# Kernel tuning notes

Hardware: AMD Instinct MI355X
Metric: run time of the kernel (lower is better)

The kernel has to match this reference:

```python
import jax, jax.numpy as jnp
import numpy as np

FACTOR = 5  # init factor


def setup_inputs() -> dict:
    key = jax.random.key(0)
    k1, k2, k3, k4 = jax.random.split(key, 4)
    B, H, L, D = 4, 8, 2048, 64
    sample_k = min(FACTOR * int(np.ceil(np.log(L))), L)  # 40
    queries = jax.random.normal(k1, (B, H, L, D), dtype=jnp.float32)
    keys = jax.random.normal(k2, (B, H, L, D), dtype=jnp.float32)
    values = jax.random.normal(k3, (B, H, L, D), dtype=jnp.float32)
    index_sample = jax.random.randint(k4, (L, sample_k), 0, L)
    return {"queries": queries, "keys": keys, "values": values,
            "index_sample": index_sample}


def reference(queries, keys, values, index_sample):
    B, H, L_Q, D = queries.shape
    L_K = keys.shape[2]
    n_top = min(FACTOR * int(np.ceil(np.log(L_Q))), L_Q)

    # --- _prob_QK ---
    # Gather sampled keys per query position: [B,H,L_Q,sample_k,D]
    K_sample = keys[:, :, index_sample, :]
    # Q.unsqueeze(3) @ K_sample^T -> [B,H,L_Q,sample_k]
    Q_K_sample = jnp.einsum('bhld,bhlsd->bhls', queries, K_sample)
    # sparsity measure M = max - mean
    M = Q_K_sample.max(axis=-1) - Q_K_sample.sum(axis=-1) / L_K
    _, M_top = jax.lax.top_k(M, n_top)  # [B,H,n_top]
    # gather top queries: [B,H,n_top,D]
    Q_reduce = jnp.take_along_axis(queries, M_top[..., None], axis=2)
    # full scores for top queries: [B,H,n_top,L_K]
    scores_top = jnp.einsum('bhud,bhkd->bhuk', Q_reduce, keys)

    # --- scale ---
    scale = 1.0 / np.sqrt(D).astype(np.float32)
    scores_top = scores_top * scale

    # --- initial context (mask_flag=False): mean of V broadcast over L_Q ---
    V_mean = values.mean(axis=2)  # [B,H,D]
    context = jnp.broadcast_to(V_mean[:, :, None, :], (B, H, L_Q, D))

    # --- update context at top-query positions ---
    attn = jax.nn.softmax(scores_top, axis=-1)           # [B,H,n_top,L_K]
    ctx_update = jnp.einsum('bhuk,bhkd->bhud', attn, values)
    b_idx = jnp.arange(B)[:, None, None]
    h_idx = jnp.arange(H)[None, :, None]
    context = context.at[b_idx, h_idx, M_top].set(ctx_update)
    return context
```

## Files before the change

### kernel.cpp

```cpp
#include <hip/hip_runtime.h>
#include <math.h>

#define BH 32
#define L  2048
#define D  64
#define SK 40
#define NT 40
#define NC 16
#define CK 128
#define SP 129
#define SCALE 0.125f

#define WS_M      0
#define WS_MTOP   262144
#define WS_VP     267264
#define WS_VM     529408
#define WS_QTOP   537600
#define WS_OPART  865280
#define WS_MPART  6108160
#define WS_LPART  6190080

template <int CTRL>
__device__ __forceinline__ float dpp_add(float x) {
    int y = __builtin_amdgcn_update_dpp(0, __float_as_int(x), CTRL, 0xF, 0xF, true);
    return x + __int_as_float(y);
}

__global__ __launch_bounds__(512) void kMV(const float* __restrict__ Q,
                                           const float* __restrict__ K,
                                           const float* __restrict__ V,
                                           const int* __restrict__ idx,
                                           float* __restrict__ M,
                                           float* __restrict__ Vp)
{
    __shared__ int   sidx[64 * SK];
    __shared__ float red[512];

    int t    = threadIdx.x;
    int b    = blockIdx.x;
    int head = ((b >> 3) & 3) * 8 + (b & 7);
    int qc   = b >> 5;
    int l0   = qc * 64;

    {
        int d = t & 63, r = t >> 6;
        const float* Vb = V + ((size_t)head * L + l0 + r * 8) * D + d;
        float acc = 0.f;
        #pragma unroll
        for (int k = 0; k < 8; ++k) acc += Vb[(size_t)k * D];
        red[t] = acc;
    }
    for (int i = t; i < 64 * SK; i += 512) sidx[i] = idx[l0 * SK + i];
    __syncthreads();
    if (t < 64) {
        float s = 0.f;
        #pragma unroll
        for (int rr = 0; rr < 8; ++rr) s += red[t + rr * 64];
        Vp[(head * 32 + qc) * 64 + t] = s;
    }

    int wave = t >> 6, lane = t & 63;
    int g  = lane >> 3;
    int dl = lane & 7;
    int lq = wave * 8 + g;
    size_t qid = (size_t)head * L + (l0 + lq);

    const float4* Q4 = reinterpret_cast<const float4*>(Q);
    float4 q0 = Q4[qid * 16 + dl * 2 + 0];
    float4 q1 = Q4[qid * 16 + dl * 2 + 1];
    const float4* Kb4 = reinterpret_cast<const float4*>(K) + (size_t)head * L * 16;

    const int* sp = sidx + lq * SK;

    float4 ka[4], kb[4];
    #pragma unroll
    for (int s = 0; s < 4; ++s) {
        const float4* kp = Kb4 + ((sp[s] << 4) + (dl << 1));
        ka[s] = kp[0]; kb[s] = kp[1];
    }
    float mx = -INFINITY, sm = 0.f;
    #pragma unroll
    for (int s = 0; s < SK; ++s) {
        float4 k0 = ka[s & 3], k1 = kb[s & 3];
        if (s + 4 < SK) {
            const float4* kp = Kb4 + ((sp[s + 4] << 4) + (dl << 1));
            ka[s & 3] = kp[0]; kb[s & 3] = kp[1];
        }
        float p = q0.x * k0.x + q0.y * k0.y + q0.z * k0.z + q0.w * k0.w
                + q1.x * k1.x + q1.y * k1.y + q1.z * k1.z + q1.w * k1.w;
        p = dpp_add<0xB1>(p);
        p = dpp_add<0x4E>(p);
        p = dpp_add<0x12C>(p);
        mx = fmaxf(mx, p);
        sm += p;
    }
    if (dl == 0) M[qid] = mx - sm * (1.0f / (float)L);
}

__global__ __launch_bounds__(256) void kTopVm(const float* __restrict__ M,
                                              const float* __restrict__ Vp,
                                              const float* __restrict__ Q,
                                              int* __restrict__ Mtop,
                                              float* __restrict__ Vm,
                                              float* __restrict__ Qtop)
{
    __shared__ unsigned int keys[L];
    __shared__ int hist[256];
    __shared__ int wtot[4];
    __shared__ unsigned int pref_s;
    __shared__ int krem_s;
    __shared__ int cnt_gt, cnt_eq;
    __shared__ int eqlist[64];
    __shared__ int stop[NT];

    int bh = blockIdx.x;
    int t  = threadIdx.x;
    int lane = t & 63, w = t >> 6;

    if (t < 64) {
        float s = 0.f;
        #pragma unroll
        for (int c = 0; c < 32; ++c) s += Vp[(bh * 32 + c) * 64 + t];
        Vm[bh * D + t] = s * (1.0f / (float)L);
    }

    for (int i = t; i < L; i += 256) {
        unsigned int u = __float_as_uint(M[bh * L + i]);
        keys[i] = (u & 0x80000000u) ? ~u : (u | 0x80000000u);
    }
    if (t == 0) { pref_s = 0u; krem_s = NT; cnt_gt = 0; cnt_eq = 0; }
    __syncthreads();

    #pragma unroll
    for (int shift = 24; shift >= 0; shift -= 8) {
        hist[t] = 0;
        __syncthreads();
        unsigned int pref = pref_s;
        int krem = krem_s;
        for (int i = t; i < L; i += 256) {
            unsigned int k  = keys[i];
            unsigned int hi = (shift == 24) ? 0u : (k >> (shift + 8));
            if (hi == pref) atomicAdd(&hist[(k >> shift) & 0xFF], 1);
        }
        __syncthreads();
        int h = hist[t];
        int v = h;
        #pragma unroll
        for (int o = 1; o < 64; o <<= 1) {
            int u = __shfl_down(v, o, 64);
            if (lane + o < 64) v += u;
        }
        if (lane == 0) wtot[w] = v;
        __syncthreads();
        int ss = v;
        #pragma unroll
        for (int w2 = 1; w2 < 4; ++w2) if (w2 > w) ss += wtot[w2];
        if (ss - h < krem && ss >= krem) {
            krem_s = krem - (ss - h);
            pref_s = (pref << 8) | (unsigned int)t;
        }
    }
    __syncthreads();

    unsigned int T = pref_s;
    int krem = krem_s;
    for (int i = t; i < L; i += 256) {
        unsigned int k = keys[i];
        if (k > T) {
            int p = atomicAdd(&cnt_gt, 1);
            Mtop[bh * NT + p] = i;
            stop[p] = i;
        } else if (k == T) {
            int p = atomicAdd(&cnt_eq, 1);
            if (p < 64) eqlist[p] = i;
        }
    }
    __syncthreads();
    if (t == 0) {
        int base = cnt_gt;
        int m = cnt_eq < 64 ? cnt_eq : 64;
        for (int q = 0; q < krem; ++q) {
            int best = 0x7fffffff, bj = -1;
            for (int j = 0; j < m; ++j) if (eqlist[j] < best) { best = eqlist[j]; bj = j; }
            Mtop[bh * NT + base + q] = best;
            stop[base + q] = best;
            if (bj >= 0) eqlist[bj] = 0x7fffffff;
        }
    }
    __syncthreads();
    const float4* Qg = reinterpret_cast<const float4*>(Q) + (size_t)bh * L * 16;
    float4* Qt = reinterpret_cast<float4*>(Qtop) + (size_t)bh * NT * 16;
    for (int i = t; i < NT * 16; i += 256)
        Qt[i] = Qg[(size_t)stop[i >> 4] * 16 + (i & 15)];
}

__global__ __launch_bounds__(256, 2) void kAttnPart(const float* __restrict__ Qtop,
                                                    const float* __restrict__ K,
                                                    const float* __restrict__ V,
                                                    const float* __restrict__ Vm,
                                                    float* __restrict__ Opart,
                                                    float* __restrict__ mpart,
                                                    float* __restrict__ lpart,
                                                    float* __restrict__ out)
{
    __shared__ float4 V4[CK * 16];
    __shared__ float  S[NT * SP];
    __shared__ float  smax[NT], ssum[NT];

    int c = blockIdx.x, bh = blockIdx.y;
    int t = threadIdx.x;

    {
        const float4* Vm4 = reinterpret_cast<const float4*>(Vm + bh * D);
        float4* outB = reinterpret_cast<float4*>(out) + ((size_t)bh * L + c * CK) * 16;
        #pragma unroll
        for (int k = 0; k < 8; ++k) { int i = t + k * 256; outB[i] = Vm4[i & 15]; }
    }

    const float4* Vg = reinterpret_cast<const float4*>(V) + ((size_t)bh * L + c * CK) * 16;
    float4 vreg[8];
    #pragma unroll
    for (int k = 0; k < 8; ++k) vreg[k] = Vg[t + k * 256];

    int w    = __builtin_amdgcn_readfirstlane(t) >> 6;
    int lane = t & 63;
    const float4* Kg = reinterpret_cast<const float4*>(K) + ((size_t)bh * L + c * CK) * 16;
    float4 k0[16], k1[16];
    #pragma unroll
    for (int d4 = 0; d4 < 16; ++d4) {
        k0[d4] = Kg[(size_t)lane * 16 + d4];
        k1[d4] = Kg[(size_t)(64 + lane) * 16 + d4];
    }

    const float* Qb = Qtop + ((size_t)bh * NT + w * 10) * D;
    float p0[10], p1[10];
    #pragma unroll
    for (int i = 0; i < 10; ++i) {
        const float* qrow = Qb + i * D;
        float a0 = 0.f, a1 = 0.f;
        #pragma unroll
        for (int d4 = 0; d4 < 16; ++d4) {
            float4 q4 = *reinterpret_cast<const float4*>(qrow + d4 * 4);
            a0 += q4.x * k0[d4].x + q4.y * k0[d4].y + q4.z * k0[d4].z + q4.w * k0[d4].w;
            a1 += q4.x * k1[d4].x + q4.y * k1[d4].y + q4.z * k1[d4].z + q4.w * k1[d4].w;
        }
        p0[i] = a0 * SCALE; p1[i] = a1 * SCALE;
    }

    #pragma unroll
    for (int i = 0; i < 10; ++i) {
        int u = w * 10 + i;
        float m = fmaxf(p0[i], p1[i]);
        #pragma unroll
        for (int o = 1; o < 64; o <<= 1) m = fmaxf(m, __shfl_xor(m, o, 64));
        float e0 = __expf(p0[i] - m), e1 = __expf(p1[i] - m);
        float l2 = e0 + e1;
        #pragma unroll
        for (int o = 1; o < 64; o <<= 1) l2 += __shfl_xor(l2, o, 64);
        S[u * SP + lane]      = e0;
        S[u * SP + 64 + lane] = e1;
        if (lane == 0) { smax[u] = m; ssum[u] = l2; }
    }

    #pragma unroll
    for (int k = 0; k < 8; ++k) {
        int i = t + k * 256;
        int j = i >> 4, d4 = i & 15;
        V4[j * 16 + (d4 ^ (j & 15))] = vreg[k];
    }
    __syncthreads();

    {
        int a = t >> 5, r = t & 31;
        int d4 = r >> 1, jh = r & 1;
        float4 acc[5];
        #pragma unroll
        for (int ui = 0; ui < 5; ++ui) acc[ui] = make_float4(0.f, 0.f, 0.f, 0.f);
        for (int jj = 0; jj < 64; ++jj) {
            int j = jh * 64 + jj;
            float4 v4 = V4[j * 16 + (d4 ^ (j & 15))];
            #pragma unroll
            for (int ui = 0; ui < 5; ++ui) {
                float p = S[(a + 8 * ui) * SP + j];
                acc[ui].x += p * v4.x; acc[ui].y += p * v4.y;
                acc[ui].z += p * v4.z; acc[ui].w += p * v4.w;
            }
        }
        #pragma unroll
        for (int ui = 0; ui < 5; ++ui) {
            acc[ui].x = dpp_add<0xB1>(acc[ui].x);
            acc[ui].y = dpp_add<0xB1>(acc[ui].y);
            acc[ui].z = dpp_add<0xB1>(acc[ui].z);
            acc[ui].w = dpp_add<0xB1>(acc[ui].w);
        }
        if (jh == 0) {
            float4* Og = reinterpret_cast<float4*>(Opart) + ((size_t)(bh * NC + c) * NT) * 16;
            #pragma unroll
            for (int ui = 0; ui < 5; ++ui)
                Og[(a + 8 * ui) * 16 + d4] = acc[ui];
        }
    }
    if (t < NT) {
        mpart[(bh * NC + c) * NT + t] = smax[t];
        lpart[(bh * NC + c) * NT + t] = ssum[t];
    }
}

__global__ __launch_bounds__(64) void kCombine(const float* __restrict__ Opart,
                                               const float* __restrict__ mpart,
                                               const float* __restrict__ lpart,
                                               const int* __restrict__ Mtop,
                                               float* __restrict__ out)
{
    int u = blockIdx.x, bh = blockIdx.y, d = threadIdx.x;
    float gm = -INFINITY, den = 0.f, o = 0.f;
    for (int c = 0; c < NC; ++c) {
        int pi = (bh * NC + c) * NT + u;
        float mv = mpart[pi], lv = lpart[pi];
        float nm = fmaxf(gm, mv);
        float r1 = __expf(gm - nm), r2 = __expf(mv - nm);
        o   = o * r1 + r2 * Opart[(size_t)pi * D + d];
        den = den * r1 + r2 * lv;
        gm  = nm;
    }
    int qrow = Mtop[bh * NT + u];
    out[((size_t)bh * L + qrow) * D + d] = o / den;
}

extern "C" void kernel_launch(void* const* d_in, const int* in_sizes, int n_in,
                              void* d_out, int out_size, void* d_ws, size_t ws_size,
                              hipStream_t stream)
{
    const float* Q   = (const float*)d_in[0];
    const float* K   = (const float*)d_in[1];
    const float* V   = (const float*)d_in[2];
    const int*   idx = (const int*)d_in[3];
    float* out = (float*)d_out;

    char* ws = (char*)d_ws;
    float* M     = (float*)(ws + WS_M);
    int*   Mtop  = (int*)  (ws + WS_MTOP);
    float* Vp    = (float*)(ws + WS_VP);
    float* Vm    = (float*)(ws + WS_VM);
    float* Qtop  = (float*)(ws + WS_QTOP);
    float* Opart = (float*)(ws + WS_OPART);
    float* mpart = (float*)(ws + WS_MPART);
    float* lpart = (float*)(ws + WS_LPART);

    kMV      <<<1024, 512, 0, stream>>>(Q, K, V, idx, M, Vp);
    kTopVm   <<<BH, 256, 0, stream>>>(M, Vp, Q, Mtop, Vm, Qtop);
    kAttnPart<<<dim3(NC, BH), 256, 0, stream>>>(Qtop, K, V, Vm, Opart, mpart, lpart, out);
    kCombine <<<dim3(NT, BH), 64, 0, stream>>>(Opart, mpart, lpart, Mtop, out);
}
```

Measured before the change: 186.9 us.

## Halve attention chunk size to double split-K blocks and simplify combine

The key chunk per attention block drops from 128 to 64 keys, so twice as many blocks run, each holding fewer registers, and the occupancy hint is removed. The combine kernel now finds the global max first and then sums weighted partials in one unrolled pass, instead of doing an online rescale at every step. The sampled-score kernel drops its manual 4-deep software prefetch in favour of a plain loop unrolled by 4. The cost is twice as many partial outputs to write and to read back during the combine.

```diff
diff --git a/kernel.cpp b/kernel.cpp
--- a/kernel.cpp
+++ b/kernel.cpp
@@ -6,9 +6,9 @@
 #define D  64
 #define SK 40
 #define NT 40
-#define NC 16
-#define CK 128
-#define SP 129
+#define NC 32
+#define CK 64
+#define SP 65
 #define SCALE 0.125f
 
 #define WS_M      0
@@ -17,8 +17,8 @@
 #define WS_VM     529408
 #define WS_QTOP   537600
 #define WS_OPART  865280
-#define WS_MPART  6108160
-#define WS_LPART  6190080
+#define WS_MPART  11351040
+#define WS_LPART  11514880
 
 template <int CTRL>
 __device__ __forceinline__ float dpp_add(float x) {
@@ -70,22 +70,12 @@
     float4 q1 = Q4[qid * 16 + dl * 2 + 1];
     const float4* Kb4 = reinterpret_cast<const float4*>(K) + (size_t)head * L * 16;
 
-    const int* sp = sidx + lq * SK;
-
-    float4 ka[4], kb[4];
-    #pragma unroll
-    for (int s = 0; s < 4; ++s) {
-        const float4* kp = Kb4 + ((sp[s] << 4) + (dl << 1));
-        ka[s] = kp[0]; kb[s] = kp[1];
-    }
     float mx = -INFINITY, sm = 0.f;
-    #pragma unroll
+    #pragma unroll 4
     for (int s = 0; s < SK; ++s) {
-        float4 k0 = ka[s & 3], k1 = kb[s & 3];
-        if (s + 4 < SK) {
-            const float4* kp = Kb4 + ((sp[s + 4] << 4) + (dl << 1));
-            ka[s & 3] = kp[0]; kb[s & 3] = kp[1];
-        }
+        int kr = sidx[lq * SK + s];
+        const float4* kp = Kb4 + (size_t)kr * 16 + dl * 2;
+        float4 k0 = kp[0], k1 = kp[1];
         float p = q0.x * k0.x + q0.y * k0.y + q0.z * k0.z + q0.w * k0.w
                 + q1.x * k1.x + q1.y * k1.y + q1.z * k1.z + q1.w * k1.w;
         p = dpp_add<0xB1>(p);
@@ -194,16 +184,16 @@
         Qt[i] = Qg[(size_t)stop[i >> 4] * 16 + (i & 15)];
 }
 
-__global__ __launch_bounds__(256, 2) void kAttnPart(const float* __restrict__ Qtop,
-                                                    const float* __restrict__ K,
-                                                    const float* __restrict__ V,
-                                                    const float* __restrict__ Vm,
-                                                    float* __restrict__ Opart,
-                                                    float* __restrict__ mpart,
-                                                    float* __restrict__ lpart,
-                                                    float* __restrict__ out)
-{
-    __shared__ float4 V4[CK * 16];
+__global__ __launch_bounds__(256) void kAttnPart(const float* __restrict__ Qtop,
+                                                 const float* __restrict__ K,
+                                                 const float* __restrict__ V,
+                                                 const float* __restrict__ Vm,
+                                                 float* __restrict__ Opart,
+                                                 float* __restrict__ mpart,
+                                                 float* __restrict__ lpart,
+                                                 float* __restrict__ out)
+{
+    __shared__ float4 V4s[CK * 16];
     __shared__ float  S[NT * SP];
     __shared__ float  smax[NT], ssum[NT];
 
@@ -214,59 +204,53 @@
         const float4* Vm4 = reinterpret_cast<const float4*>(Vm + bh * D);
         float4* outB = reinterpret_cast<float4*>(out) + ((size_t)bh * L + c * CK) * 16;
         #pragma unroll
-        for (int k = 0; k < 8; ++k) { int i = t + k * 256; outB[i] = Vm4[i & 15]; }
+        for (int k = 0; k < 4; ++k) { int i = t + k * 256; outB[i] = Vm4[i & 15]; }
     }
 
     const float4* Vg = reinterpret_cast<const float4*>(V) + ((size_t)bh * L + c * CK) * 16;
-    float4 vreg[8];
-    #pragma unroll
-    for (int k = 0; k < 8; ++k) vreg[k] = Vg[t + k * 256];
+    float4 vreg[4];
+    #pragma unroll
+    for (int k = 0; k < 4; ++k) vreg[k] = Vg[t + k * 256];
 
     int w    = __builtin_amdgcn_readfirstlane(t) >> 6;
     int lane = t & 63;
     const float4* Kg = reinterpret_cast<const float4*>(K) + ((size_t)bh * L + c * CK) * 16;
-    float4 k0[16], k1[16];
-    #pragma unroll
-    for (int d4 = 0; d4 < 16; ++d4) {
-        k0[d4] = Kg[(size_t)lane * 16 + d4];
-        k1[d4] = Kg[(size_t)(64 + lane) * 16 + d4];
-    }
-
-    const float* Qb = Qtop + ((size_t)bh * NT + w * 10) * D;
-    float p0[10], p1[10];
+    float4 k[16];
+    #pragma unroll
+    for (int d4 = 0; d4 < 16; ++d4) k[d4] = Kg[(size_t)lane * 16 + d4];
+
+    const float4* Qb = reinterpret_cast<const float4*>(Qtop) + ((size_t)bh * NT + w * 10) * 16;
+    float p[10];
     #pragma unroll
     for (int i = 0; i < 10; ++i) {
-        const float* qrow = Qb + i * D;
-        float a0 = 0.f, a1 = 0.f;
+        float a0 = 0.f;
         #pragma unroll
         for (int d4 = 0; d4 < 16; ++d4) {
-            float4 q4 = *reinterpret_cast<const float4*>(qrow + d4 * 4);
-            a0 += q4.x * k0[d4].x + q4.y * k0[d4].y + q4.z * k0[d4].z + q4.w * k0[d4].w;
-            a1 += q4.x * k1[d4].x + q4.y * k1[d4].y + q4.z * k1[d4].z + q4.w * k1[d4].w;
-        }
-        p0[i] = a0 * SCALE; p1[i] = a1 * SCALE;
+            float4 q4 = Qb[i * 16 + d4];
+            a0 += q4.x * k[d4].x + q4.y * k[d4].y + q4.z * k[d4].z + q4.w * k[d4].w;
+        }
+        p[i] = a0 * SCALE;
     }
 
     #pragma unroll
     for (int i = 0; i < 10; ++i) {
         int u = w * 10 + i;
-        float m = fmaxf(p0[i], p1[i]);
+        float m = p[i];
         #pragma unroll
         for (int o = 1; o < 64; o <<= 1) m = fmaxf(m, __shfl_xor(m, o, 64));
-        float e0 = __expf(p0[i] - m), e1 = __expf(p1[i] - m);
-        float l2 = e0 + e1;
+        float e = __expf(p[i] - m);
+        float l2 = e;
         #pragma unroll
         for (int o = 1; o < 64; o <<= 1) l2 += __shfl_xor(l2, o, 64);
-        S[u * SP + lane]      = e0;
-        S[u * SP + 64 + lane] = e1;
+        S[u * SP + lane] = e;
         if (lane == 0) { smax[u] = m; ssum[u] = l2; }
     }
 
     #pragma unroll
-    for (int k = 0; k < 8; ++k) {
-        int i = t + k * 256;
+    for (int kk = 0; kk < 4; ++kk) {
+        int i = t + kk * 256;
         int j = i >> 4, d4 = i & 15;
-        V4[j * 16 + (d4 ^ (j & 15))] = vreg[k];
+        V4s[j * 16 + (d4 ^ (j & 15))] = vreg[kk];
     }
     __syncthreads();
 
@@ -276,14 +260,14 @@
         float4 acc[5];
         #pragma unroll
         for (int ui = 0; ui < 5; ++ui) acc[ui] = make_float4(0.f, 0.f, 0.f, 0.f);
-        for (int jj = 0; jj < 64; ++jj) {
-            int j = jh * 64 + jj;
-            float4 v4 = V4[j * 16 + (d4 ^ (j & 15))];
+        for (int jj = 0; jj < 32; ++jj) {
+            int j = jh * 32 + jj;
+            float4 v4 = V4s[j * 16 + (d4 ^ (j & 15))];
             #pragma unroll
             for (int ui = 0; ui < 5; ++ui) {
-                float p = S[(a + 8 * ui) * SP + j];
-                acc[ui].x += p * v4.x; acc[ui].y += p * v4.y;
-                acc[ui].z += p * v4.z; acc[ui].w += p * v4.w;
+                float pw = S[(a + 8 * ui) * SP + j];
+                acc[ui].x += pw * v4.x; acc[ui].y += pw * v4.y;
+                acc[ui].z += pw * v4.z; acc[ui].w += pw * v4.w;
             }
         }
         #pragma unroll
@@ -313,15 +297,16 @@
                                                float* __restrict__ out)
 {
     int u = blockIdx.x, bh = blockIdx.y, d = threadIdx.x;
-    float gm = -INFINITY, den = 0.f, o = 0.f;
+    float gm = -INFINITY;
+    #pragma unroll
+    for (int c = 0; c < NC; ++c) gm = fmaxf(gm, mpart[(bh * NC + c) * NT + u]);
+    float den = 0.f, o = 0.f;
+    #pragma unroll
     for (int c = 0; c < NC; ++c) {
         int pi = (bh * NC + c) * NT + u;
-        float mv = mpart[pi], lv = lpart[pi];
-        float nm = fmaxf(gm, mv);
-        float r1 = __expf(gm - nm), r2 = __expf(mv - nm);
-        o   = o * r1 + r2 * Opart[(size_t)pi * D + d];
-        den = den * r1 + r2 * lv;
-        gm  = nm;
+        float wgt = __expf(mpart[pi] - gm);
+        den += wgt * lpart[pi];
+        o   += wgt * Opart[(size_t)pi * D + d];
     }
     int qrow = Mtop[bh * NT + u];
     out[((size_t)bh * L + qrow) * D + d] = o / den;
```

Measured after the change: 164.4 us. 1.14x faster.
